# Kernel tuning notes

Hardware: AMD Instinct MI355X
Metric: run time of the kernel (lower is better)

## Reference

```python
import jax, jax.numpy as jnp
import numpy as np

N_NODES = 50000
N_EDGES = 800000
D = 128        # input_dim == output_dim
D_EDGE = 64    # edge_attr_size
Z_DIM = 2 * D + D_EDGE  # 320


def setup_inputs() -> dict:
    key = jax.random.key(0)
    k1, k2, k3, k4, k5 = jax.random.split(key, 5)
    x = jax.random.normal(k1, (N_NODES, D), dtype=jnp.float32)
    edge_index = jax.random.randint(k2, (2, N_EDGES), 0, N_NODES, dtype=jnp.int64)
    edge_attr = jax.random.normal(k3, (N_EDGES, D_EDGE), dtype=jnp.float32)
    scale = 1.0 / np.sqrt(Z_DIM)
    W_f = jax.random.normal(k4, (Z_DIM, D), dtype=jnp.float32) * scale
    W_s = jax.random.normal(k5, (Z_DIM, D), dtype=jnp.float32) * scale
    b_f = jnp.zeros((D,), dtype=jnp.float32)
    b_s = jnp.zeros((D,), dtype=jnp.float32)
    return {"x": x, "edge_index": edge_index, "edge_attr": edge_attr,
            "W_f": W_f, "b_f": b_f, "W_s": W_s, "b_s": b_s}


def reference(x, edge_index, edge_attr, W_f, b_f, W_s, b_s):
    # Dropout(p=0.0) is identity in inference.
    src = edge_index[0]  # j (message source)
    dst = edge_index[1]  # i (message target)
    # z_e = [x_i, x_j, e_ij]  -> [E, 2D + D_edge]
    z = jnp.concatenate([x[dst], x[src], edge_attr], axis=-1)
    # CGConv message: sigmoid(lin_f(z)) * softplus(lin_s(z))
    msg = jax.nn.sigmoid(z @ W_f + b_f) * jax.nn.softplus(z @ W_s + b_s)
    # scatter-add aggregation + residual
    out = jax.ops.segment_sum(msg, dst, num_segments=x.shape[0]) + x
    # use_activation=True -> ReLU
    return jax.nn.relu(out)
```

## Files before the change

kernel.cpp:

```cpp
#include <hip/hip_runtime.h>
#include <hip/hip_bf16.h>

#define E_TOTAL   800000
#define NN        50000
#define DD        128
#define DE        64
#define ZDIM      320
#define KE        192
#define MT        64
#define NBS       196

typedef short bf16x8 __attribute__((ext_vector_type(8)));
typedef float f32x4  __attribute__((ext_vector_type(4)));

__device__ __forceinline__ unsigned short f2bf(float f) {
    union { float f; unsigned int u; } v; v.f = f;
    unsigned int u = v.u;
    return (unsigned short)((u + 0x7fffu + ((u >> 16) & 1u)) >> 16);
}

__device__ __forceinline__ float bf2f(unsigned short h) {
    union { unsigned u; float f; } v; v.u = ((unsigned)h) << 16; return v.f;
}

__device__ __forceinline__ unsigned pkbf2(float a, float b) {
    __hip_bfloat162 h = __float22bfloat162_rn(make_float2(a, b));
    unsigned u; __builtin_memcpy(&u, &h, 4); return u;
}

__device__ __forceinline__ uint2 pkbf4(float4 v) {
    uint2 r; r.x = pkbf2(v.x, v.y); r.y = pkbf2(v.z, v.w); return r;
}

__device__ __forceinline__ float fast_rcp(float x) {
#if __has_builtin(__builtin_amdgcn_rcpf)
    return __builtin_amdgcn_rcpf(x);
#else
    return 1.0f / x;
#endif
}


__global__ void scan_part(const int* __restrict__ counts, int* __restrict__ partial) {
    __shared__ int red[256];
    int t = threadIdx.x, k = blockIdx.x * 256 + t;
    red[t] = (k < NN) ? counts[k] : 0;
    __syncthreads();
    for (int d = 128; d > 0; d >>= 1) {
        if (t < d) red[t] += red[t + d];
        __syncthreads();
    }
    if (t == 0) partial[blockIdx.x] = red[0];
}

__global__ void scan_top(int* __restrict__ partial) {
    __shared__ int s[256];
    int t = threadIdx.x;
    int v = (t < NBS) ? partial[t] : 0;
    s[t] = v; __syncthreads();
    for (int d = 1; d < 256; d <<= 1) {
        int a = (t >= d) ? s[t - d] : 0;
        __syncthreads();
        s[t] += a;
        __syncthreads();
    }
    if (t < NBS) partial[t] = s[t] - v;
}

__global__ void scan_final(const int* __restrict__ counts,
                           const int* __restrict__ partial,
                           int* __restrict__ cursor) {
    __shared__ int s[256];
    int t = threadIdx.x, k = blockIdx.x * 256 + t;
    int v = (k < NN) ? counts[k] : 0;
    s[t] = v; __syncthreads();
    for (int d = 1; d < 256; d <<= 1) {
        int a = (t >= d) ? s[t - d] : 0;
        __syncthreads();
        s[t] += a;
        __syncthreads();
    }
    if (k < NN) cursor[k] = partial[blockIdx.x] + s[t] - v;
}

__global__ void scatter_kernel(const int* __restrict__ ei, int* __restrict__ cursor,
                               uint2* __restrict__ spak2) {
    int e = blockIdx.x * 256 + threadIdx.x;
    if (e < E_TOTAL) {
        int d = ei[E_TOTAL + e];
        int pos = atomicAdd(&cursor[d], 1);
        uint2 p; p.x = ((unsigned)d << 16) | (unsigned)ei[e]; p.y = (unsigned)e;
        spak2[pos] = p;
    }
}


__global__ void prep_kernel2(const float* __restrict__ x,
                             const int* __restrict__ ei,
                             const float* __restrict__ W_f,
                             const float* __restrict__ W_s,
                             unsigned short* __restrict__ WtE,
                             unsigned short* __restrict__ WtN,
                             int* __restrict__ counts,
                             float* __restrict__ out) {
    int id = blockIdx.x * 256 + threadIdx.x;
    ((float4*)out)[id] = ((const float4*)x)[id];
    if (id < E_TOTAL) atomicAdd(&counts[ei[E_TOTAL + id]], 1);
    if (id < 256 * DE) {
        int n = id >> 6, k = id & 63;
        int ok = 2 * DD + k;
        float wv = (n < DD) ? W_f[ok * DD + n] : W_s[ok * DD + (n - DD)];
        WtE[id] = f2bf(wv);
    } else if (id < 256 * DE + 2 * 256 * DD) {
        int id2 = id - 256 * DE;
        int part = id2 >> 15;
        int r = id2 & 32767;
        int n = r >> 7, k = r & 127;
        int ok = part * DD + k;
        float wv = (n < DD) ? W_f[ok * DD + n] : W_s[ok * DD + (n - DD)];
        WtN[id2] = f2bf(wv);
    }
}

__global__ __launch_bounds__(256, 4)
void node_kernel2(const float* __restrict__ x,
                  const unsigned short* __restrict__ WtN,
                  const float* __restrict__ bf_, const float* __restrict__ bs_,
                  unsigned int* __restrict__ nodeP32) {
    __shared__ unsigned short A_lds[MT * DD];
    const int t = threadIdx.x;
    const int m_off = blockIdx.x * MT;
    const int part = blockIdx.y;
    const int lane = t & 63, w = t >> 6, l15 = lane & 15, quad = lane >> 4;

    #pragma unroll
    for (int it = 0; it < 8; ++it) {
        int idx = it * 256 + t;
        int e = idx >> 5, kq = idx & 31;
        int row = m_off + e; if (row >= NN) row = NN - 1;
        float4 v = ((const float4*)(x + (size_t)row * DD))[kq];
        int g = kq >> 1;
        int col = ((g & ~7) | ((g & 7) ^ (e & 7))) * 8 + (kq & 1) * 4;
        *((uint2*)&A_lds[e * DD + col]) = pkbf4(v);
    }

    f32x4 acc[4][4] = {};
    const int nt0 = 2 * w;
    const unsigned short* Bp[4];
    #pragma unroll
    for (int u = 0; u < 4; ++u) {
        int nt = nt0 + ((u < 2) ? u : (6 + u));
        Bp[u] = WtN + (size_t)part * (256 * DD) +
                (size_t)(nt * 16 + l15) * DD + quad * 8;
    }
    __syncthreads();

    #pragma unroll
    for (int ks = 0; ks < 4; ++ks) {
        bf16x8 af[4], bfr[4];
        #pragma unroll
        for (int i = 0; i < 4; ++i) {
            int m = i * 16 + l15;
            int g = 4 * ks + quad;
            int col = ((g & ~7) | ((g & 7) ^ (l15 & 7))) * 8;
            af[i] = *((const bf16x8*)&A_lds[m * DD + col]);
        }
        #pragma unroll
        for (int u = 0; u < 4; ++u)
            bfr[u] = *((const bf16x8*)(Bp[u] + ks * 32));
        #pragma unroll
        for (int i = 0; i < 4; ++i)
            #pragma unroll
            for (int u = 0; u < 4; ++u)
                acc[i][u] = __builtin_amdgcn_mfma_f32_16x16x32_bf16(
                    af[i], bfr[u], acc[i][u], 0, 0, 0);
    }

    const int c0 = 32 * w + l15, c1 = c0 + 16;
    const float bf0 = part ? 0.f : bf_[c0], bs0 = part ? 0.f : bs_[c0];
    const float bf1 = part ? 0.f : bf_[c1], bs1 = part ? 0.f : bs_[c1];
    #pragma unroll
    for (int i = 0; i < 4; ++i)
        #pragma unroll
        for (int j = 0; j < 4; ++j) {
            int e = i * 16 + quad * 4 + j;
            int row = m_off + e;
            if (row < NN) {
                unsigned int* np = nodeP32 + (size_t)row * 256 + part * 128;
                np[c0] = pkbf2(acc[i][0][j] + bf0, acc[i][2][j] + bs0);
                np[c1] = pkbf2(acc[i][1][j] + bf1, acc[i][3][j] + bs1);
            }
        }
}

__global__ __launch_bounds__(512, 4)
void edge_kernel2(const float* __restrict__ ea,
                  const unsigned short* __restrict__ WtE,
                  const unsigned int* __restrict__ nodeP32,
                  float* __restrict__ out,
                  const uint2* __restrict__ spak2) {
    __shared__ float sumb[MT][DD];
    __shared__ unsigned short A_lds[MT * DE];
    __shared__ int dst_lds[MT];
    __shared__ int src_lds[MT];
    __shared__ int eid_lds[MT];
    __shared__ int runid_lds[MT];
    __shared__ int rdst_lds[MT];
    __shared__ int rbound_lds[MT];
    __shared__ int ndist_lds;

    const int t = threadIdx.x;
    const int m_off = blockIdx.x * MT;
    const int lane = t & 63, w2 = t >> 6, l15 = lane & 15, quad = lane >> 4;

    if (t < MT) {
        uint2 p = spak2[m_off + t];
        int dsv = (int)(p.x >> 16);
        dst_lds[t] = dsv;
        src_lds[t] = (int)(p.x & 0xffffu);
        eid_lds[t] = (int)p.y;
        int updsv = __shfl_up(dsv, 1);
        int flag = (t == 0 || dsv != updsv) ? 1 : 0;
        unsigned long long m = __ballot(flag != 0);
        int rid = __popcll(m << (63 - t)) - 1;
        runid_lds[t] = rid;
        if (flag) { rdst_lds[rid] = dsv; rbound_lds[rid] = 0; }
        int nd = __popcll(m);
        if (t == 0) {
            ndist_lds = nd;
            if (m_off > 0 &&
                (int)(spak2[m_off - 1].x >> 16) == dsv)
                rbound_lds[0] = 1;
        }
        if (t == MT - 1) {
            if (m_off + MT < E_TOTAL &&
                (int)(spak2[m_off + MT].x >> 16) == dsv)
                rbound_lds[nd - 1] = 1;
        }
    }
    __syncthreads();

    const int c = 16 * w2 + l15;

    float4 va[2];
    #pragma unroll
    for (int it = 0; it < 2; ++it) {
        int idx = it * 512 + t;
        int e = idx >> 4;
        va[it] = ((const float4*)(ea + (size_t)eid_lds[e] * DE))[idx & 15];
    }
    unsigned int ps[16], pd[16];
    #pragma unroll
    for (int i = 0; i < 4; ++i)
        #pragma unroll
        for (int j = 0; j < 4; ++j) {
            int e = i * 16 + quad * 4 + j;
            ps[i * 4 + j] = nodeP32[(size_t)src_lds[e] * 256 + 128 + c];
            pd[i * 4 + j] = nodeP32[(size_t)dst_lds[e] * 256 + c];
        }
    {
        int nd = ndist_lds;
        int col = t & 127, rb = t >> 7;
        for (int r = rb; r < nd; r += 4) sumb[r][col] = 0.f;
    }
    #pragma unroll
    for (int it = 0; it < 2; ++it) {
        int idx = it * 512 + t;
        int e = idx >> 4, kq = idx & 15;
        int g = kq >> 1;
        int col = ((g & 7) ^ (e & 7)) * 8 + (kq & 1) * 4;
        *((uint2*)&A_lds[e * DE + col]) = pkbf4(va[it]);
    }

    f32x4 acc[4][2] = {};
    const unsigned short* Bp[2];
    #pragma unroll
    for (int u = 0; u < 2; ++u) {
        int nt = w2 + u * 8;
        Bp[u] = WtE + (size_t)(nt * 16 + l15) * DE + quad * 8;
    }
    __syncthreads();

    #pragma unroll
    for (int ks = 0; ks < 2; ++ks) {
        bf16x8 af[4], bfr[2];
        #pragma unroll
        for (int i = 0; i < 4; ++i) {
            int m = i * 16 + l15;
            int g = 4 * ks + quad;
            int col = ((g & 7) ^ (l15 & 7)) * 8;
            af[i] = *((const bf16x8*)&A_lds[m * DE + col]);
        }
        #pragma unroll
        for (int u = 0; u < 2; ++u)
            bfr[u] = *((const bf16x8*)(Bp[u] + ks * 32));
        #pragma unroll
        for (int i = 0; i < 4; ++i)
            #pragma unroll
            for (int u = 0; u < 2; ++u)
                acc[i][u] = __builtin_amdgcn_mfma_f32_16x16x32_bf16(
                    af[i], bfr[u], acc[i][u], 0, 0, 0);
    }

    int rprev = -1;
    float s0 = 0.f, nf = 0.f, ns = 0.f;
    #pragma unroll
    for (int i = 0; i < 4; ++i)
        #pragma unroll
        for (int j = 0; j < 4; ++j) {
            int e = i * 16 + quad * 4 + j;
            int rid = runid_lds[e];
            if (rid != rprev) {
                if (rprev >= 0) atomicAdd(&sumb[rprev][c], s0);
                rprev = rid; s0 = 0.f;
                unsigned int pk = pd[i * 4 + j];
                nf = bf2f((unsigned short)(pk & 0xffffu));
                ns = bf2f((unsigned short)(pk >> 16));
            }
            unsigned int pp = ps[i * 4 + j];
            float f  = acc[i][0][j] + nf + bf2f((unsigned short)(pp & 0xffffu));
            float sg = acc[i][1][j] + ns + bf2f((unsigned short)(pp >> 16));
            s0 += fast_rcp(1.f + __expf(-f)) *
                  (fmaxf(sg, 0.f) + __logf(1.f + __expf(-fabsf(sg))));
        }
    atomicAdd(&sumb[rprev][c], s0);
    __syncthreads();

    {
        int nd = ndist_lds;
        int col = t & 127, rb = t >> 7;
        for (int r = rb; r < nd; r += 4) {
            float v = sumb[r][col];
            float* op = out + (size_t)rdst_lds[r] * DD + col;
            if (rbound_lds[r]) atomicAdd(op, v);
            else *op += v;
        }
    }
}


__global__ void prep_kernel(const float* __restrict__ x,
                            const int* __restrict__ ei,
                            const float* __restrict__ W_f,
                            const float* __restrict__ W_s,
                            unsigned short* __restrict__ WtE,
                            unsigned short* __restrict__ WtN,
                            int* __restrict__ counts,
                            float* __restrict__ out) {
    int id = blockIdx.x * 256 + threadIdx.x;
    ((float4*)out)[id] = ((const float4*)x)[id];
    if (id < E_TOTAL) atomicAdd(&counts[ei[E_TOTAL + id]], 1);
    if (id < 256 * KE) {
        int n = id / KE, k = id - n * KE;
        int ok = 128 + k;
        float wv = (n < DD) ? W_f[ok * DD + n] : W_s[ok * DD + (n - DD)];
        WtE[id] = f2bf(wv);
    } else if (id < 256 * KE + 256 * DD) {
        int id2 = id - 256 * KE;
        int n = id2 / DD, k = id2 - n * DD;
        float wv = (n < DD) ? W_f[k * DD + n] : W_s[k * DD + (n - DD)];
        WtN[id2] = f2bf(wv);
    }
}

__global__ __launch_bounds__(256, 4)
void node_kernel(const float* __restrict__ x,
                 const unsigned short* __restrict__ WtN,
                 const float* __restrict__ bf_, const float* __restrict__ bs_,
                 unsigned short* __restrict__ nodeP) {
    __shared__ unsigned short A_lds[MT * DD];
    const int t = threadIdx.x;
    const int m_off = blockIdx.x * MT;
    const int lane = t & 63, w = t >> 6, l15 = lane & 15, quad = lane >> 4;

    #pragma unroll
    for (int it = 0; it < 8; ++it) {
        int idx = it * 256 + t;
        int e = idx >> 5, kq = idx & 31;
        int row = m_off + e; if (row >= NN) row = NN - 1;
        float4 v = ((const float4*)(x + (size_t)row * DD))[kq];
        int g = kq >> 1;
        int col = ((g & ~7) | ((g & 7) ^ (e & 7))) * 8 + (kq & 1) * 4;
        *((uint2*)&A_lds[e * DD + col]) = pkbf4(v);
    }

    f32x4 acc[4][4] = {};
    const int nt0 = 2 * w;
    const unsigned short* Bp[4];
    #pragma unroll
    for (int u = 0; u < 4; ++u) {
        int nt = nt0 + ((u < 2) ? u : (6 + u));
        Bp[u] = WtN + (size_t)(nt * 16 + l15) * DD + quad * 8;
    }
    __syncthreads();

    #pragma unroll
    for (int ks = 0; ks < 4; ++ks) {
        bf16x8 af[4], bfr[4];
        #pragma unroll
        for (int i = 0; i < 4; ++i) {
            int m = i * 16 + l15;
            int g = 4 * ks + quad;
            int col = ((g & ~7) | ((g & 7) ^ (l15 & 7))) * 8;
            af[i] = *((const bf16x8*)&A_lds[m * DD + col]);
        }
        #pragma unroll
        for (int u = 0; u < 4; ++u)
            bfr[u] = *((const bf16x8*)(Bp[u] + ks * 32));
        #pragma unroll
        for (int i = 0; i < 4; ++i)
            #pragma unroll
            for (int u = 0; u < 4; ++u)
                acc[i][u] = __builtin_amdgcn_mfma_f32_16x16x32_bf16(
                    af[i], bfr[u], acc[i][u], 0, 0, 0);
    }

    const int c0 = 32 * w + l15, c1 = c0 + 16;
    const float bf0 = bf_[c0], bs0 = bs_[c0], bf1 = bf_[c1], bs1 = bs_[c1];
    #pragma unroll
    for (int i = 0; i < 4; ++i)
        #pragma unroll
        for (int j = 0; j < 4; ++j) {
            int e = i * 16 + quad * 4 + j;
            int row = m_off + e;
            if (row < NN) {
                uint2 pk;
                pk.x = pkbf2(acc[i][0][j] + bf0, acc[i][1][j] + bf1);
                pk.y = pkbf2(acc[i][2][j] + bs0, acc[i][3][j] + bs1);
                *((uint2*)(nodeP + (size_t)row * 256 + w * 64 + l15 * 4)) = pk;
            }
        }
}

__global__ __launch_bounds__(256, 4)
void edge_kernel(const float* __restrict__ x,
                 const float* __restrict__ ea,
                 const unsigned short* __restrict__ WtE,
                 const unsigned short* __restrict__ nodeP,
                 float* __restrict__ out,
                 const uint2* __restrict__ spak2) {
    __shared__ unsigned short A_lds[MT * KE];
    __shared__ int dst_lds[MT];
    __shared__ int src_lds[MT];
    __shared__ int eid_lds[MT];

    const int t = threadIdx.x;
    const int m_off = blockIdx.x * MT;
    const int lane = t & 63, w = t >> 6, l15 = lane & 15, quad = lane >> 4;

    if (t < MT) {
        uint2 p = spak2[m_off + t];
        dst_lds[t] = (int)(p.x >> 16);
        src_lds[t] = (int)(p.x & 0xffffu);
        eid_lds[t] = (int)p.y;
    }
    __syncthreads();

    #pragma unroll
    for (int it = 0; it < 4; ++it) {
        int idx = it * 256 + t;
        int e = idx >> 4, kq = idx & 15;
        float4 v = ((const float4*)(ea + (size_t)eid_lds[e] * DE))[kq];
        int g = 16 + (kq >> 1);
        int col = ((g & ~7) | ((g & 7) ^ (e & 7))) * 8 + (kq & 1) * 4;
        *((uint2*)&A_lds[e * KE + col]) = pkbf4(v);
    }
    #pragma unroll
    for (int it = 0; it < 8; ++it) {
        int idx = it * 256 + t;
        int e = idx >> 5, kq = idx & 31;
        float4 v = ((const float4*)(x + (size_t)src_lds[e] * DD))[kq];
        int g = kq >> 1;
        int col = ((g & ~7) | ((g & 7) ^ (e & 7))) * 8 + (kq & 1) * 4;
        *((uint2*)&A_lds[e * KE + col]) = pkbf4(v);
    }

    f32x4 acc[4][4] = {};
    const int nt0 = 2 * w;
    const unsigned short* Bp[4];
    #pragma unroll
    for (int u = 0; u < 4; ++u) {
        int nt = nt0 + ((u < 2) ? u : (6 + u));
        Bp[u] = WtE + (size_t)(nt * 16 + l15) * KE + quad * 8;
    }
    __syncthreads();

    #pragma unroll
    for (int ks = 0; ks < 6; ++ks) {
        bf16x8 af[4], bfr[4];
        #pragma unroll
        for (int i = 0; i < 4; ++i) {
            int m = i * 16 + l15;
            int g = 4 * ks + quad;
            int col = ((g & ~7) | ((g & 7) ^ (l15 & 7))) * 8;
            af[i] = *((const bf16x8*)&A_lds[m * KE + col]);
        }
        #pragma unroll
        for (int u = 0; u < 4; ++u)
            bfr[u] = *((const bf16x8*)(Bp[u] + ks * 32));
        #pragma unroll
        for (int i = 0; i < 4; ++i)
            #pragma unroll
            for (int u = 0; u < 4; ++u)
                acc[i][u] = __builtin_amdgcn_mfma_f32_16x16x32_bf16(
                    af[i], bfr[u], acc[i][u], 0, 0, 0);
    }

    const int c0 = 32 * w + l15, c1 = c0 + 16;
    const int np_off = w * 64 + l15 * 4;

    int d = -1;
    float s0 = 0.f, s1 = 0.f, nf0 = 0.f, ns0 = 0.f, nf1 = 0.f, ns1 = 0.f;
    #pragma unroll
    for (int i = 0; i < 4; ++i)
        #pragma unroll
        for (int j = 0; j < 4; ++j) {
            int e = i * 16 + quad * 4 + j;
            int dd = dst_lds[e];
            if (dd != d) {
                if (d >= 0) {
                    atomicAdd(out + (size_t)d * DD + c0, s0);
                    atomicAdd(out + (size_t)d * DD + c1, s1);
                }
                d = dd; s0 = 0.f; s1 = 0.f;
                uint2 pk = *((const uint2*)(nodeP + (size_t)d * 256 + np_off));
                nf0 = bf2f((unsigned short)(pk.x & 0xffffu));
                nf1 = bf2f((unsigned short)(pk.x >> 16));
                ns0 = bf2f((unsigned short)(pk.y & 0xffffu));
                ns1 = bf2f((unsigned short)(pk.y >> 16));
            }
            float f0  = acc[i][0][j] + nf0;
            float sg0 = acc[i][2][j] + ns0;
            s0 += fast_rcp(1.f + __expf(-f0)) *
                  (fmaxf(sg0, 0.f) + __logf(1.f + __expf(-fabsf(sg0))));
            float f1  = acc[i][1][j] + nf1;
            float sg1 = acc[i][3][j] + ns1;
            s1 += fast_rcp(1.f + __expf(-f1)) *
                  (fmaxf(sg1, 0.f) + __logf(1.f + __expf(-fabsf(sg1))));
        }
    atomicAdd(out + (size_t)d * DD + c0, s0);
    atomicAdd(out + (size_t)d * DD + c1, s1);
}

__global__ void relu_kernel(float* __restrict__ out) {
    int id = blockIdx.x * 256 + threadIdx.x;
    if (id < NN * DD / 4) {
        float4 v = ((float4*)out)[id];
        v.x = fmaxf(v.x, 0.0f); v.y = fmaxf(v.y, 0.0f);
        v.z = fmaxf(v.z, 0.0f); v.w = fmaxf(v.w, 0.0f);
        ((float4*)out)[id] = v;
    }
}


__global__ void prep_fb(const float* __restrict__ x,
                        const float* __restrict__ W_f,
                        const float* __restrict__ W_s,
                        unsigned short* __restrict__ Wt,
                        float* __restrict__ out) {
    int id = blockIdx.x * 256 + threadIdx.x;
    if (id < NN * DD / 4)
        ((float4*)out)[id] = ((const float4*)x)[id];
    if (id < 2 * DD * ZDIM) {
        int n = id / ZDIM, k = id - n * ZDIM;
        float wv = (n < DD) ? W_f[k * DD + n] : W_s[k * DD + (n - DD)];
        Wt[n * ZDIM + k] = f2bf(wv);
    }
}

__global__ __launch_bounds__(256, 3)
void edge_fb(const float* __restrict__ x,
             const int* __restrict__ ei,
             const float* __restrict__ ea,
             const unsigned short* __restrict__ Wt,
             const float* __restrict__ bf_,
             const float* __restrict__ bs_,
             float* __restrict__ out) {
    __shared__ unsigned short A_lds[MT * ZDIM];
    __shared__ int dst_lds[MT];
    __shared__ int src_lds[MT];

    const int t = threadIdx.x;
    const int m_off = blockIdx.x * MT;
    const int lane = t & 63, w = t >> 6, l15 = lane & 15, quad = lane >> 4;

    if (t < MT) dst_lds[t] = ei[E_TOTAL + m_off + t];
    else if (t < 2 * MT) src_lds[t - MT] = ei[m_off + (t - MT)];
    __syncthreads();

    #pragma unroll
    for (int it = 0; it < 4; ++it) {
        int idx = it * 256 + t;
        int e = idx >> 4, kq = idx & 15;
        float4 v = ((const float4*)(ea + (size_t)(m_off + e) * DE))[kq];
        int g = 32 + (kq >> 1);
        int col = ((g & ~7) | ((g & 7) ^ (e & 7))) * 8 + (kq & 1) * 4;
        *((uint2*)&A_lds[e * ZDIM + col]) = pkbf4(v);
    }
    #pragma unroll
    for (int it = 0; it < 8; ++it) {
        int idx = it * 256 + t;
        int e = idx >> 5, kq = idx & 31;
        float4 v = ((const float4*)(x + (size_t)dst_lds[e] * DD))[kq];
        int g = kq >> 1;
        int col = ((g & ~7) | ((g & 7) ^ (e & 7))) * 8 + (kq & 1) * 4;
        *((uint2*)&A_lds[e * ZDIM + col]) = pkbf4(v);
    }
    #pragma unroll
    for (int it = 0; it < 8; ++it) {
        int idx = it * 256 + t;
        int e = idx >> 5, kq = idx & 31;
        float4 v = ((const float4*)(x + (size_t)src_lds[e] * DD))[kq];
        int g = 16 + (kq >> 1);
        int col = ((g & ~7) | ((g & 7) ^ (e & 7))) * 8 + (kq & 1) * 4;
        *((uint2*)&A_lds[e * ZDIM + col]) = pkbf4(v);
    }

    f32x4 acc[4][4] = {};
    const int nt0 = 2 * w;
    const unsigned short* Bp[4];
    #pragma unroll
    for (int u = 0; u < 4; ++u) {
        int nt = nt0 + ((u < 2) ? u : (6 + u));
        Bp[u] = Wt + (size_t)(nt * 16 + l15) * ZDIM + quad * 8;
    }
    __syncthreads();

    #pragma unroll
    for (int ks = 0; ks < 10; ++ks) {
        bf16x8 af[4], bfr[4];
        #pragma unroll
        for (int i = 0; i < 4; ++i) {
            int m = i * 16 + l15;
            int g = 4 * ks + quad;
            int col = ((g & ~7) | ((g & 7) ^ (l15 & 7))) * 8;
            af[i] = *((const bf16x8*)&A_lds[m * ZDIM + col]);
        }
        #pragma unroll
        for (int u = 0; u < 4; ++u)
            bfr[u] = *((const bf16x8*)(Bp[u] + ks * 32));
        #pragma unroll
        for (int i = 0; i < 4; ++i)
            #pragma unroll
            for (int u = 0; u < 4; ++u)
                acc[i][u] = __builtin_amdgcn_mfma_f32_16x16x32_bf16(
                    af[i], bfr[u], acc[i][u], 0, 0, 0);
    }

    const int c0 = 32 * w + l15, c1 = c0 + 16;
    const float bf0 = bf_[c0], bs0 = bs_[c0], bf1 = bf_[c1], bs1 = bs_[c1];
    #pragma unroll
    for (int i = 0; i < 4; ++i)
        #pragma unroll
        for (int j = 0; j < 4; ++j) {
            int e = i * 16 + quad * 4 + j;
            float* op = out + (size_t)dst_lds[e] * DD;
            float f0 = acc[i][0][j] + bf0;
            float sg0 = acc[i][2][j] + bs0;
            atomicAdd(op + c0, fast_rcp(1.f + __expf(-f0)) *
                (fmaxf(sg0, 0.f) + __logf(1.f + __expf(-fabsf(sg0)))));
            float f1 = acc[i][1][j] + bf1;
            float sg1 = acc[i][3][j] + bs1;
            atomicAdd(op + c1, fast_rcp(1.f + __expf(-f1)) *
                (fmaxf(sg1, 0.f) + __logf(1.f + __expf(-fabsf(sg1)))));
        }
}


extern "C" void kernel_launch(void* const* d_in, const int* in_sizes, int n_in,
                              void* d_out, int out_size, void* d_ws, size_t ws_size,
                              hipStream_t stream) {
    (void)in_sizes; (void)n_in; (void)out_size;
    const float* x   = (const float*)d_in[0];
    const int*   ei  = (const int*)d_in[1];
    const float* ea  = (const float*)d_in[2];
    const float* W_f = (const float*)d_in[3];
    const float* b_f = (const float*)d_in[4];
    const float* W_s = (const float*)d_in[5];
    const float* b_s = (const float*)d_in[6];
    float* out = (float*)d_out;

    char* ws = (char*)d_ws;
    const size_t WS_NEED2 = 58164864;
    const size_t WS_NEED1 = 32564864;

    if (ws_size >= WS_NEED2) {
        unsigned short* WtE2   = (unsigned short*)ws;
        unsigned short* WtN2   = (unsigned short*)(ws + 32768);
        int*            counts = (int*)(ws + 163840);
        int*            cursor = (int*)(ws + 363840);
        int*            partial= (int*)(ws + 563840);
        uint2*          spak2  = (uint2*)(ws + 564864);
        unsigned int*   nodeP32= (unsigned int*)(ws + 6964864);

        hipMemsetAsync(counts, 0, NN * sizeof(int), stream);
        prep_kernel2<<<NN * DD / 4 / 256, 256, 0, stream>>>(
            x, ei, W_f, W_s, WtE2, WtN2, counts, out);
        scan_part<<<NBS, 256, 0, stream>>>(counts, partial);
        scan_top<<<1, 256, 0, stream>>>(partial);
        scan_final<<<NBS, 256, 0, stream>>>(counts, partial, cursor);
        scatter_kernel<<<(E_TOTAL + 255) / 256, 256, 0, stream>>>(ei, cursor, spak2);
        dim3 ng((NN + MT - 1) / MT, 2);
        node_kernel2<<<ng, 256, 0, stream>>>(x, WtN2, b_f, b_s, nodeP32);
        edge_kernel2<<<E_TOTAL / MT, 512, 0, stream>>>(
            ea, WtE2, nodeP32, out, spak2);
    } else if (ws_size >= WS_NEED1) {
        unsigned short* WtE    = (unsigned short*)ws;
        unsigned short* WtN    = (unsigned short*)(ws + 98304);
        int*            counts = (int*)(ws + 163840);
        int*            cursor = (int*)(ws + 363840);
        int*            partial= (int*)(ws + 563840);
        uint2*          spak2  = (uint2*)(ws + 564864);
        unsigned short* nodeP  = (unsigned short*)(ws + 6964864);

        hipMemsetAsync(counts, 0, NN * sizeof(int), stream);
        prep_kernel<<<NN * DD / 4 / 256, 256, 0, stream>>>(
            x, ei, W_f, W_s, WtE, WtN, counts, out);
        scan_part<<<NBS, 256, 0, stream>>>(counts, partial);
        scan_top<<<1, 256, 0, stream>>>(partial);
        scan_final<<<NBS, 256, 0, stream>>>(counts, partial, cursor);
        scatter_kernel<<<(E_TOTAL + 255) / 256, 256, 0, stream>>>(ei, cursor, spak2);
        node_kernel<<<(NN + MT - 1) / MT, 256, 0, stream>>>(x, WtN, b_f, b_s, nodeP);
        edge_kernel<<<E_TOTAL / MT, 256, 0, stream>>>(
            x, ea, WtE, nodeP, out, spak2);
    } else {
        unsigned short* Wt = (unsigned short*)ws;
        prep_fb<<<6250, 256, 0, stream>>>(x, W_f, W_s, Wt, out);
        edge_fb<<<E_TOTAL / MT, 256, 0, stream>>>(x, ei, ea, Wt, b_f, b_s, out);
    }

    relu_kernel<<<6250, 256, 0, stream>>>(out);
}
```

Measured before the change: 606.7 us.

## Pipeline edge tiles per block with double-buffered gathers and a separate aggregation buffer

Adds a new path where each edge block handles four 64-edge tiles. The edge-attribute loads and node-projection gathers for the next tile are issued while the current tile runs its MFMA and epilogue, using double-buffered LDS. Aggregation goes to a zeroed workspace buffer, which a final kernel combines with x and applies ReLU. This removes the x copy into out and merges the scan top and final steps into one kernel. The path needs a larger workspace, uses more registers, and uses fewer blocks, so the hidden latency may be offset by lower occupancy.

New measurement: 706.1 us. +16.4%, slower.

```diff
diff --git a/kernel.cpp b/kernel.cpp
--- a/kernel.cpp
+++ b/kernel.cpp
@@ -6,8 +6,8 @@
 #define DD        128
 #define DE        64
 #define ZDIM      320
-#define KE        192
 #define MT        64
+#define NTPB      4
 #define NBS       196
 
 typedef short bf16x8 __attribute__((ext_vector_type(8)));
@@ -38,6 +38,13 @@
 #else
     return 1.0f / x;
 #endif
+}
+
+__device__ __forceinline__ void barrier_lgkm() {
+    __builtin_amdgcn_sched_barrier(0);
+    asm volatile("s_waitcnt lgkmcnt(0)" ::: "memory");
+    __builtin_amdgcn_s_barrier();
+    __builtin_amdgcn_sched_barrier(0);
 }
 
 
@@ -83,6 +90,31 @@
     if (k < NN) cursor[k] = partial[blockIdx.x] + s[t] - v;
 }
 
+__global__ void scan_final2(const int* __restrict__ counts,
+                            const int* __restrict__ partial,
+                            int* __restrict__ cursor) {
+    __shared__ int s[256], p2[256], orig[256];
+    int t = threadIdx.x, k = blockIdx.x * 256 + t;
+    int pv = (t < NBS) ? partial[t] : 0;
+    p2[t] = pv; orig[t] = pv; __syncthreads();
+    for (int d = 1; d < 256; d <<= 1) {
+        int a = (t >= d) ? p2[t - d] : 0;
+        __syncthreads();
+        p2[t] += a;
+        __syncthreads();
+    }
+    int blkoff = p2[blockIdx.x] - orig[blockIdx.x];
+    int v = (k < NN) ? counts[k] : 0;
+    s[t] = v; __syncthreads();
+    for (int d = 1; d < 256; d <<= 1) {
+        int a = (t >= d) ? s[t - d] : 0;
+        __syncthreads();
+        s[t] += a;
+        __syncthreads();
+    }
+    if (k < NN) cursor[k] = blkoff + s[t] - v;
+}
+
 __global__ void scatter_kernel(const int* __restrict__ ei, int* __restrict__ cursor,
                                uint2* __restrict__ spak2) {
     int e = blockIdx.x * 256 + threadIdx.x;
@@ -91,6 +123,314 @@
         int pos = atomicAdd(&cursor[d], 1);
         uint2 p; p.x = ((unsigned)d << 16) | (unsigned)ei[e]; p.y = (unsigned)e;
         spak2[pos] = p;
+    }
+}
+
+
+__global__ void prep_kernel4(const int* __restrict__ ei,
+                             const float* __restrict__ W_f,
+                             const float* __restrict__ W_s,
+                             unsigned short* __restrict__ WtE,
+                             unsigned short* __restrict__ WtN,
+                             int* __restrict__ counts,
+                             float* __restrict__ aggr) {
+    int id = blockIdx.x * 256 + threadIdx.x;
+    float4 z; z.x = 0.f; z.y = 0.f; z.z = 0.f; z.w = 0.f;
+    ((float4*)aggr)[id] = z;
+    if (id < E_TOTAL) atomicAdd(&counts[ei[E_TOTAL + id]], 1);
+    if (id < 256 * DE) {
+        int n = id >> 6, k = id & 63;
+        int ok = 2 * DD + k;
+        float wv = (n < DD) ? W_f[ok * DD + n] : W_s[ok * DD + (n - DD)];
+        WtE[id] = f2bf(wv);
+    } else if (id < 256 * DE + 2 * 256 * DD) {
+        int id2 = id - 256 * DE;
+        int part = id2 >> 15;
+        int r = id2 & 32767;
+        int n = r >> 7, k = r & 127;
+        int ok = part * DD + k;
+        float wv = (n < DD) ? W_f[ok * DD + n] : W_s[ok * DD + (n - DD)];
+        WtN[id2] = f2bf(wv);
+    }
+}
+
+__global__ __launch_bounds__(512, 4)
+void node_kernel3(const float* __restrict__ x,
+                  const unsigned short* __restrict__ WtN,
+                  const float* __restrict__ bf_, const float* __restrict__ bs_,
+                  unsigned int* __restrict__ nodeP32) {
+    __shared__ unsigned short A_lds[MT * DD];
+    const int t = threadIdx.x;
+    const int m_off = blockIdx.x * MT;
+    const int lane = t & 63, w8 = t >> 6;
+    const int part = w8 >> 2, w = w8 & 3;
+    const int l15 = lane & 15, quad = lane >> 4;
+
+    #pragma unroll
+    for (int it = 0; it < 4; ++it) {
+        int idx = it * 512 + t;
+        int e = idx >> 5, kq = idx & 31;
+        int row = m_off + e; if (row >= NN) row = NN - 1;
+        float4 v = ((const float4*)(x + (size_t)row * DD))[kq];
+        int g = kq >> 1;
+        int col = ((g & ~7) | ((g & 7) ^ (e & 7))) * 8 + (kq & 1) * 4;
+        *((uint2*)&A_lds[e * DD + col]) = pkbf4(v);
+    }
+
+    f32x4 acc[4][4] = {};
+    const int nt0 = 2 * w;
+    const unsigned short* Bp[4];
+    #pragma unroll
+    for (int u = 0; u < 4; ++u) {
+        int nt = nt0 + ((u < 2) ? u : (6 + u));
+        Bp[u] = WtN + (size_t)part * (256 * DD) +
+                (size_t)(nt * 16 + l15) * DD + quad * 8;
+    }
+    __syncthreads();
+
+    #pragma unroll
+    for (int ks = 0; ks < 4; ++ks) {
+        bf16x8 af[4], bfr[4];
+        #pragma unroll
+        for (int i = 0; i < 4; ++i) {
+            int m = i * 16 + l15;
+            int g = 4 * ks + quad;
+            int col = ((g & ~7) | ((g & 7) ^ (l15 & 7))) * 8;
+            af[i] = *((const bf16x8*)&A_lds[m * DD + col]);
+        }
+        #pragma unroll
+        for (int u = 0; u < 4; ++u)
+            bfr[u] = *((const bf16x8*)(Bp[u] + ks * 32));
+        #pragma unroll
+        for (int i = 0; i < 4; ++i)
+            #pragma unroll
+            for (int u = 0; u < 4; ++u)
+                acc[i][u] = __builtin_amdgcn_mfma_f32_16x16x32_bf16(
+                    af[i], bfr[u], acc[i][u], 0, 0, 0);
+    }
+
+    const int c0 = 32 * w + l15, c1 = c0 + 16;
+    const float bf0 = part ? 0.f : bf_[c0], bs0 = part ? 0.f : bs_[c0];
+    const float bf1 = part ? 0.f : bf_[c1], bs1 = part ? 0.f : bs_[c1];
+    #pragma unroll
+    for (int i = 0; i < 4; ++i)
+        #pragma unroll
+        for (int j = 0; j < 4; ++j) {
+            int e = i * 16 + quad * 4 + j;
+            int row = m_off + e;
+            if (row < NN) {
+                unsigned int* np = nodeP32 + (size_t)row * 256 + part * 128;
+                np[c0] = pkbf2(acc[i][0][j] + bf0, acc[i][2][j] + bs0);
+                np[c1] = pkbf2(acc[i][1][j] + bf1, acc[i][3][j] + bs1);
+            }
+        }
+}
+
+
+#define ISSUE_VA(VA, K)                                                        \
+    _Pragma("unroll")                                                          \
+    for (int it = 0; it < 2; ++it) {                                           \
+        int idx = it * 512 + t;                                                \
+        int e = idx >> 4;                                                      \
+        VA[it] = ((const float4*)(ea + (size_t)eid_lds[K][e] * DE))[idx & 15]; \
+    }
+
+#define ISSUE_GATHER(PS, PD, K)                                                \
+    _Pragma("unroll")                                                          \
+    for (int i = 0; i < 4; ++i)                                                \
+        _Pragma("unroll")                                                      \
+        for (int j = 0; j < 4; ++j) {                                          \
+            int e = i * 16 + quad * 4 + j;                                     \
+            PS[i * 4 + j] = nodeP32[(size_t)src_lds[K][e] * 256 + 128 + c];    \
+            PD[i * 4 + j] = nodeP32[(size_t)dst_lds[K][e] * 256 + c];          \
+        }
+
+#define STORE_A(VA, BUF)                                                       \
+    _Pragma("unroll")                                                          \
+    for (int it = 0; it < 2; ++it) {                                           \
+        int idx = it * 512 + t;                                                \
+        int e = idx >> 4, kq = idx & 15;                                       \
+        int colx = (((kq >> 1) & 7) ^ (e & 7)) * 8 + (kq & 1) * 4;             \
+        *((uint2*)&A_lds[BUF][e * DE + colx]) = pkbf4(VA[it]);                 \
+    }
+
+#define ZERO_ACC                                                               \
+    { f32x4 zz = {};                                                           \
+      _Pragma("unroll")                                                        \
+      for (int i = 0; i < 4; ++i) { acc[i][0] = zz; acc[i][1] = zz; } }
+
+#define GEMM_T(BUF)                                                            \
+    _Pragma("unroll")                                                          \
+    for (int ks = 0; ks < 2; ++ks) {                                           \
+        bf16x8 af[4];                                                          \
+        _Pragma("unroll")                                                      \
+        for (int i = 0; i < 4; ++i) {                                          \
+            int m = i * 16 + l15;                                              \
+            int g = 4 * ks + quad;                                             \
+            int colx = ((g & 7) ^ (l15 & 7)) * 8;                              \
+            af[i] = *((const bf16x8*)&A_lds[BUF][m * DE + colx]);              \
+        }                                                                      \
+        _Pragma("unroll")                                                      \
+        for (int i = 0; i < 4; ++i) {                                          \
+            acc[i][0] = __builtin_amdgcn_mfma_f32_16x16x32_bf16(               \
+                af[i], bfr[0][ks], acc[i][0], 0, 0, 0);                        \
+            acc[i][1] = __builtin_amdgcn_mfma_f32_16x16x32_bf16(               \
+                af[i], bfr[1][ks], acc[i][1], 0, 0, 0);                        \
+        }                                                                      \
+    }
+
+#define EPILOG(PS, PD, K)                                                      \
+    {                                                                          \
+        int rprev = -1; float s0 = 0.f, nf = 0.f, ns = 0.f;                    \
+        _Pragma("unroll")                                                      \
+        for (int i = 0; i < 4; ++i)                                            \
+            _Pragma("unroll")                                                  \
+            for (int j = 0; j < 4; ++j) {                                      \
+                int e = i * 16 + quad * 4 + j;                                 \
+                int rid = runid_lds[K][e];                                     \
+                if (rid != rprev) {                                            \
+                    if (rprev >= 0) atomicAdd(&sumb[rprev][c], s0);            \
+                    rprev = rid; s0 = 0.f;                                     \
+                    unsigned pk = PD[i * 4 + j];                               \
+                    nf = bf2f((unsigned short)(pk & 0xffffu));                 \
+                    ns = bf2f((unsigned short)(pk >> 16));                     \
+                }                                                              \
+                unsigned pp = PS[i * 4 + j];                                   \
+                float f  = acc[i][0][j] + nf + bf2f((unsigned short)(pp & 0xffffu)); \
+                float sg = acc[i][1][j] + ns + bf2f((unsigned short)(pp >> 16));     \
+                s0 += fast_rcp(1.f + __expf(-f)) *                             \
+                      (fmaxf(sg, 0.f) + __logf(1.f + __expf(-fabsf(sg))));     \
+            }                                                                  \
+        atomicAdd(&sumb[rprev][c], s0);                                        \
+    }
+
+#define WRITEOUT(K)                                                            \
+    {                                                                          \
+        int ndk = nd_lds[K];                                                   \
+        int col = t & 127, rb = t >> 7;                                        \
+        for (int r = rb; r < ndk; r += 4) {                                    \
+            float v = sumb[r][col];                                            \
+            sumb[r][col] = 0.f;                                                \
+            float* op = aggr + (size_t)rdst_lds[K][r] * DD + col;              \
+            if (rbound_lds[K][r]) atomicAdd(op, v);                            \
+            else *op = v;                                                      \
+        }                                                                      \
+    }
+
+__global__ __launch_bounds__(512, 3)
+void edge_kernel4(const float* __restrict__ ea,
+                  const unsigned short* __restrict__ WtE,
+                  const unsigned int* __restrict__ nodeP32,
+                  float* __restrict__ aggr,
+                  const uint2* __restrict__ spak2) {
+    __shared__ float sumb[MT][DD];
+    __shared__ alignas(16) unsigned short A_lds[2][MT * DE];
+    __shared__ int dst_lds[NTPB][MT];
+    __shared__ int src_lds[NTPB][MT];
+    __shared__ int eid_lds[NTPB][MT];
+    __shared__ int runid_lds[NTPB][MT];
+    __shared__ int rdst_lds[NTPB][MT];
+    __shared__ int rbound_lds[NTPB][MT];
+    __shared__ int nd_lds[NTPB];
+
+    const int t = threadIdx.x;
+    const int blk_e0 = blockIdx.x * (MT * NTPB);
+    const int lane = t & 63, w2 = t >> 6, l15 = lane & 15, quad = lane >> 4;
+    const int c = 16 * w2 + l15;
+
+    bf16x8 bfr[2][2];
+    #pragma unroll
+    for (int u = 0; u < 2; ++u) {
+        int nt = w2 + u * 8;
+        const unsigned short* bp = WtE + (size_t)(nt * 16 + l15) * DE + quad * 8;
+        bfr[u][0] = *((const bf16x8*)bp);
+        bfr[u][1] = *((const bf16x8*)(bp + 32));
+    }
+
+    if (w2 < NTPB) {
+        int tb = blk_e0 + w2 * MT;
+        uint2 p = spak2[tb + lane];
+        int dsv = (int)(p.x >> 16);
+        dst_lds[w2][lane] = dsv;
+        src_lds[w2][lane] = (int)(p.x & 0xffffu);
+        eid_lds[w2][lane] = (int)p.y;
+        int updsv = __shfl_up(dsv, 1);
+        int flag = (lane == 0 || dsv != updsv) ? 1 : 0;
+        unsigned long long m = __ballot(flag != 0);
+        int rid = __popcll(m << (63 - lane)) - 1;
+        runid_lds[w2][lane] = rid;
+        if (flag) { rdst_lds[w2][rid] = dsv; rbound_lds[w2][rid] = 0; }
+        int ndv = __popcll(m);
+        if (lane == 0) {
+            nd_lds[w2] = ndv;
+            if (tb > 0 && (int)(spak2[tb - 1].x >> 16) == dsv)
+                rbound_lds[w2][0] = 1;
+        }
+        if (lane == MT - 1) {
+            if (tb + MT < E_TOTAL && (int)(spak2[tb + MT].x >> 16) == dsv)
+                rbound_lds[w2][ndv - 1] = 1;
+        }
+    }
+    {
+        int col = t & 127, rb = t >> 7;
+        #pragma unroll
+        for (int r = rb; r < MT; r += 4) sumb[r][col] = 0.f;
+    }
+    __syncthreads();
+
+    float4 vaA[2], vaB[2];
+    unsigned psA[16], psB[16], pdA[16], pdB[16];
+    f32x4 acc[4][2];
+
+    ISSUE_VA(vaA, 0)
+    ISSUE_GATHER(psA, pdA, 0)
+    STORE_A(vaA, 0)
+    ISSUE_VA(vaB, 1)
+    ISSUE_GATHER(psB, pdB, 1)
+    barrier_lgkm();
+
+    ZERO_ACC GEMM_T(0)
+    EPILOG(psA, pdA, 0)
+    ISSUE_VA(vaA, 2)
+    ISSUE_GATHER(psA, pdA, 2)
+    STORE_A(vaB, 1)
+    barrier_lgkm();
+    WRITEOUT(0)
+    barrier_lgkm();
+
+    ZERO_ACC GEMM_T(1)
+    EPILOG(psB, pdB, 1)
+    ISSUE_VA(vaB, 3)
+    ISSUE_GATHER(psB, pdB, 3)
+    STORE_A(vaA, 0)
+    barrier_lgkm();
+    WRITEOUT(1)
+    barrier_lgkm();
+
+    ZERO_ACC GEMM_T(0)
+    EPILOG(psA, pdA, 2)
+    STORE_A(vaB, 1)
+    barrier_lgkm();
+    WRITEOUT(2)
+    barrier_lgkm();
+
+    ZERO_ACC GEMM_T(1)
+    EPILOG(psB, pdB, 3)
+    barrier_lgkm();
+    WRITEOUT(3)
+}
+
+__global__ void relu_kernel4(const float* __restrict__ x,
+                             const float* __restrict__ aggr,
+                             float* __restrict__ out) {
+    int id = blockIdx.x * 256 + threadIdx.x;
+    if (id < NN * DD / 4) {
+        float4 xv = ((const float4*)x)[id];
+        float4 av = ((const float4*)aggr)[id];
+        float4 v;
+        v.x = fmaxf(xv.x + av.x, 0.0f); v.y = fmaxf(xv.y + av.y, 0.0f);
+        v.z = fmaxf(xv.z + av.z, 0.0f); v.w = fmaxf(xv.w + av.w, 0.0f);
+        ((float4*)out)[id] = v;
     }
 }
 
@@ -228,8 +568,7 @@
         int nd = __popcll(m);
         if (t == 0) {
             ndist_lds = nd;
-            if (m_off > 0 &&
-                (int)(spak2[m_off - 1].x >> 16) == dsv)
+            if (m_off > 0 && (int)(spak2[m_off - 1].x >> 16) == dsv)
                 rbound_lds[0] = 1;
         }
         if (t == MT - 1) {
@@ -338,210 +677,6 @@
     }
 }
 
-
-__global__ void prep_kernel(const float* __restrict__ x,
-                            const int* __restrict__ ei,
-                            const float* __restrict__ W_f,
-                            const float* __restrict__ W_s,
-                            unsigned short* __restrict__ WtE,
-                            unsigned short* __restrict__ WtN,
-                            int* __restrict__ counts,
-                            float* __restrict__ out) {
-    int id = blockIdx.x * 256 + threadIdx.x;
-    ((float4*)out)[id] = ((const float4*)x)[id];
-    if (id < E_TOTAL) atomicAdd(&counts[ei[E_TOTAL + id]], 1);
-    if (id < 256 * KE) {
-        int n = id / KE, k = id - n * KE;
-        int ok = 128 + k;
-        float wv = (n < DD) ? W_f[ok * DD + n] : W_s[ok * DD + (n - DD)];
-        WtE[id] = f2bf(wv);
-    } else if (id < 256 * KE + 256 * DD) {
-        int id2 = id - 256 * KE;
-        int n = id2 / DD, k = id2 - n * DD;
-        float wv = (n < DD) ? W_f[k * DD + n] : W_s[k * DD + (n - DD)];
-        WtN[id2] = f2bf(wv);
-    }
-}
-
-__global__ __launch_bounds__(256, 4)
-void node_kernel(const float* __restrict__ x,
-                 const unsigned short* __restrict__ WtN,
-                 const float* __restrict__ bf_, const float* __restrict__ bs_,
-                 unsigned short* __restrict__ nodeP) {
-    __shared__ unsigned short A_lds[MT * DD];
-    const int t = threadIdx.x;
-    const int m_off = blockIdx.x * MT;
-    const int lane = t & 63, w = t >> 6, l15 = lane & 15, quad = lane >> 4;
-
-    #pragma unroll
-    for (int it = 0; it < 8; ++it) {
-        int idx = it * 256 + t;
-        int e = idx >> 5, kq = idx & 31;
-        int row = m_off + e; if (row >= NN) row = NN - 1;
-        float4 v = ((const float4*)(x + (size_t)row * DD))[kq];
-        int g = kq >> 1;
-        int col = ((g & ~7) | ((g & 7) ^ (e & 7))) * 8 + (kq & 1) * 4;
-        *((uint2*)&A_lds[e * DD + col]) = pkbf4(v);
-    }
-
-    f32x4 acc[4][4] = {};
-    const int nt0 = 2 * w;
-    const unsigned short* Bp[4];
-    #pragma unroll
-    for (int u = 0; u < 4; ++u) {
-        int nt = nt0 + ((u < 2) ? u : (6 + u));
-        Bp[u] = WtN + (size_t)(nt * 16 + l15) * DD + quad * 8;
-    }
-    __syncthreads();
-
-    #pragma unroll
-    for (int ks = 0; ks < 4; ++ks) {
-        bf16x8 af[4], bfr[4];
-        #pragma unroll
-        for (int i = 0; i < 4; ++i) {
-            int m = i * 16 + l15;
-            int g = 4 * ks + quad;
-            int col = ((g & ~7) | ((g & 7) ^ (l15 & 7))) * 8;
-            af[i] = *((const bf16x8*)&A_lds[m * DD + col]);
-        }
-        #pragma unroll
-        for (int u = 0; u < 4; ++u)
-            bfr[u] = *((const bf16x8*)(Bp[u] + ks * 32));
-        #pragma unroll
-        for (int i = 0; i < 4; ++i)
-            #pragma unroll
-            for (int u = 0; u < 4; ++u)
-                acc[i][u] = __builtin_amdgcn_mfma_f32_16x16x32_bf16(
-                    af[i], bfr[u], acc[i][u], 0, 0, 0);
-    }
-
-    const int c0 = 32 * w + l15, c1 = c0 + 16;
-    const float bf0 = bf_[c0], bs0 = bs_[c0], bf1 = bf_[c1], bs1 = bs_[c1];
-    #pragma unroll
-    for (int i = 0; i < 4; ++i)
-        #pragma unroll
-        for (int j = 0; j < 4; ++j) {
-            int e = i * 16 + quad * 4 + j;
-            int row = m_off + e;
-            if (row < NN) {
-                uint2 pk;
-                pk.x = pkbf2(acc[i][0][j] + bf0, acc[i][1][j] + bf1);
-                pk.y = pkbf2(acc[i][2][j] + bs0, acc[i][3][j] + bs1);
-                *((uint2*)(nodeP + (size_t)row * 256 + w * 64 + l15 * 4)) = pk;
-            }
-        }
-}
-
-__global__ __launch_bounds__(256, 4)
-void edge_kernel(const float* __restrict__ x,
-                 const float* __restrict__ ea,
-                 const unsigned short* __restrict__ WtE,
-                 const unsigned short* __restrict__ nodeP,
-                 float* __restrict__ out,
-                 const uint2* __restrict__ spak2) {
-    __shared__ unsigned short A_lds[MT * KE];
-    __shared__ int dst_lds[MT];
-    __shared__ int src_lds[MT];
-    __shared__ int eid_lds[MT];
-
-    const int t = threadIdx.x;
-    const int m_off = blockIdx.x * MT;
-    const int lane = t & 63, w = t >> 6, l15 = lane & 15, quad = lane >> 4;
-
-    if (t < MT) {
-        uint2 p = spak2[m_off + t];
-        dst_lds[t] = (int)(p.x >> 16);
-        src_lds[t] = (int)(p.x & 0xffffu);
-        eid_lds[t] = (int)p.y;
-    }
-    __syncthreads();
-
-    #pragma unroll
-    for (int it = 0; it < 4; ++it) {
-        int idx = it * 256 + t;
-        int e = idx >> 4, kq = idx & 15;
-        float4 v = ((const float4*)(ea + (size_t)eid_lds[e] * DE))[kq];
-        int g = 16 + (kq >> 1);
-        int col = ((g & ~7) | ((g & 7) ^ (e & 7))) * 8 + (kq & 1) * 4;
-        *((uint2*)&A_lds[e * KE + col]) = pkbf4(v);
-    }
-    #pragma unroll
-    for (int it = 0; it < 8; ++it) {
-        int idx = it * 256 + t;
-        int e = idx >> 5, kq = idx & 31;
-        float4 v = ((const float4*)(x + (size_t)src_lds[e] * DD))[kq];
-        int g = kq >> 1;
-        int col = ((g & ~7) | ((g & 7) ^ (e & 7))) * 8 + (kq & 1) * 4;
-        *((uint2*)&A_lds[e * KE + col]) = pkbf4(v);
-    }
-
-    f32x4 acc[4][4] = {};
-    const int nt0 = 2 * w;
-    const unsigned short* Bp[4];
-    #pragma unroll
-    for (int u = 0; u < 4; ++u) {
-        int nt = nt0 + ((u < 2) ? u : (6 + u));
-        Bp[u] = WtE + (size_t)(nt * 16 + l15) * KE + quad * 8;
-    }
-    __syncthreads();
-
-    #pragma unroll
-    for (int ks = 0; ks < 6; ++ks) {
-        bf16x8 af[4], bfr[4];
-        #pragma unroll
-        for (int i = 0; i < 4; ++i) {
-            int m = i * 16 + l15;
-            int g = 4 * ks + quad;
-            int col = ((g & ~7) | ((g & 7) ^ (l15 & 7))) * 8;
-            af[i] = *((const bf16x8*)&A_lds[m * KE + col]);
-        }
-        #pragma unroll
-        for (int u = 0; u < 4; ++u)
-            bfr[u] = *((const bf16x8*)(Bp[u] + ks * 32));
-        #pragma unroll
-        for (int i = 0; i < 4; ++i)
-            #pragma unroll
-            for (int u = 0; u < 4; ++u)
-                acc[i][u] = __builtin_amdgcn_mfma_f32_16x16x32_bf16(
-                    af[i], bfr[u], acc[i][u], 0, 0, 0);
-    }
-
-    const int c0 = 32 * w + l15, c1 = c0 + 16;
-    const int np_off = w * 64 + l15 * 4;
-
-    int d = -1;
-    float s0 = 0.f, s1 = 0.f, nf0 = 0.f, ns0 = 0.f, nf1 = 0.f, ns1 = 0.f;
-    #pragma unroll
-    for (int i = 0; i < 4; ++i)
-        #pragma unroll
-        for (int j = 0; j < 4; ++j) {
-            int e = i * 16 + quad * 4 + j;
-            int dd = dst_lds[e];
-            if (dd != d) {
-                if (d >= 0) {
-                    atomicAdd(out + (size_t)d * DD + c0, s0);
-                    atomicAdd(out + (size_t)d * DD + c1, s1);
-                }
-                d = dd; s0 = 0.f; s1 = 0.f;
-                uint2 pk = *((const uint2*)(nodeP + (size_t)d * 256 + np_off));
-                nf0 = bf2f((unsigned short)(pk.x & 0xffffu));
-                nf1 = bf2f((unsigned short)(pk.x >> 16));
-                ns0 = bf2f((unsigned short)(pk.y & 0xffffu));
-                ns1 = bf2f((unsigned short)(pk.y >> 16));
-            }
-            float f0  = acc[i][0][j] + nf0;
-            float sg0 = acc[i][2][j] + ns0;
-            s0 += fast_rcp(1.f + __expf(-f0)) *
-                  (fmaxf(sg0, 0.f) + __logf(1.f + __expf(-fabsf(sg0))));
-            float f1  = acc[i][1][j] + nf1;
-            float sg1 = acc[i][3][j] + ns1;
-            s1 += fast_rcp(1.f + __expf(-f1)) *
-                  (fmaxf(sg1, 0.f) + __logf(1.f + __expf(-fabsf(sg1))));
-        }
-    atomicAdd(out + (size_t)d * DD + c0, s0);
-    atomicAdd(out + (size_t)d * DD + c1, s1);
-}
-
 __global__ void relu_kernel(float* __restrict__ out) {
     int id = blockIdx.x * 256 + threadIdx.x;
     if (id < NN * DD / 4) {
@@ -681,10 +816,31 @@
     float* out = (float*)d_out;
 
     char* ws = (char*)d_ws;
+    const size_t WS_NEED4 = 83764864;
     const size_t WS_NEED2 = 58164864;
-    const size_t WS_NEED1 = 32564864;
-
-    if (ws_size >= WS_NEED2) {
+
+    if (ws_size >= WS_NEED4) {
+        unsigned short* WtE2   = (unsigned short*)ws;
+        unsigned short* WtN2   = (unsigned short*)(ws + 32768);
+        int*            counts = (int*)(ws + 163840);
+        int*            cursor = (int*)(ws + 363840);
+        int*            partial= (int*)(ws + 563840);
+        uint2*          spak2  = (uint2*)(ws + 564864);
+        unsigned int*   nodeP32= (unsigned int*)(ws + 6964864);
+        float*          aggr   = (float*)(ws + 58164864);
+
+        hipMemsetAsync(counts, 0, NN * sizeof(int), stream);
+        prep_kernel4<<<NN * DD / 4 / 256, 256, 0, stream>>>(
+            ei, W_f, W_s, WtE2, WtN2, counts, aggr);
+        scan_part<<<NBS, 256, 0, stream>>>(counts, partial);
+        scan_final2<<<NBS, 256, 0, stream>>>(counts, partial, cursor);
+        scatter_kernel<<<(E_TOTAL + 255) / 256, 256, 0, stream>>>(ei, cursor, spak2);
+        node_kernel3<<<(NN + MT - 1) / MT, 512, 0, stream>>>(
+            x, WtN2, b_f, b_s, nodeP32);
+        edge_kernel4<<<E_TOTAL / (MT * NTPB), 512, 0, stream>>>(
+            ea, WtE2, nodeP32, aggr, spak2);
+        relu_kernel4<<<6250, 256, 0, stream>>>(x, aggr, out);
+    } else if (ws_size >= WS_NEED2) {
         unsigned short* WtE2   = (unsigned short*)ws;
         unsigned short* WtN2   = (unsigned short*)(ws + 32768);
         int*            counts = (int*)(ws + 163840);
@@ -704,30 +860,11 @@
         node_kernel2<<<ng, 256, 0, stream>>>(x, WtN2, b_f, b_s, nodeP32);
         edge_kernel2<<<E_TOTAL / MT, 512, 0, stream>>>(
             ea, WtE2, nodeP32, out, spak2);
-    } else if (ws_size >= WS_NEED1) {
-        unsigned short* WtE    = (unsigned short*)ws;
-        unsigned short* WtN    = (unsigned short*)(ws + 98304);
-        int*            counts = (int*)(ws + 163840);
-        int*            cursor = (int*)(ws + 363840);
-        int*            partial= (int*)(ws + 563840);
-        uint2*          spak2  = (uint2*)(ws + 564864);
-        unsigned short* nodeP  = (unsigned short*)(ws + 6964864);
-
-        hipMemsetAsync(counts, 0, NN * sizeof(int), stream);
-        prep_kernel<<<NN * DD / 4 / 256, 256, 0, stream>>>(
-            x, ei, W_f, W_s, WtE, WtN, counts, out);
-        scan_part<<<NBS, 256, 0, stream>>>(counts, partial);
-        scan_top<<<1, 256, 0, stream>>>(partial);
-        scan_final<<<NBS, 256, 0, stream>>>(counts, partial, cursor);
-        scatter_kernel<<<(E_TOTAL + 255) / 256, 256, 0, stream>>>(ei, cursor, spak2);
-        node_kernel<<<(NN + MT - 1) / MT, 256, 0, stream>>>(x, WtN, b_f, b_s, nodeP);
-        edge_kernel<<<E_TOTAL / MT, 256, 0, stream>>>(
-            x, ea, WtE, nodeP, out, spak2);
+        relu_kernel<<<6250, 256, 0, stream>>>(out);
     } else {
         unsigned short* Wt = (unsigned short*)ws;
         prep_fb<<<6250, 256, 0, stream>>>(x, W_f, W_s, Wt, out);
         edge_fb<<<E_TOTAL / MT, 256, 0, stream>>>(x, ei, ea, Wt, b_f, b_s, out);
-    }
-
-    relu_kernel<<<6250, 256, 0, stream>>>(out);
-}
+        relu_kernel<<<6250, 256, 0, stream>>>(out);
+    }
+}
```
